# Kernel optimization log

Hardware: AMD Instinct MI355X
Metric: run time of the kernel (lower is better)

Reference implementation:

```python
import jax, jax.numpy as jnp
import numpy as np

KS = (16, 16, 16)  # k per layer

def _knn_idx(pts, k):
    # pts: (P, C). Exclude self (knn_graph default loop=False).
    P = pts.shape[0]
    sq = jnp.sum(pts * pts, axis=1)
    d2 = sq[:, None] + sq[None, :] - 2.0 * (pts @ pts.T)  # (P, P)
    d2 = d2.at[jnp.arange(P), jnp.arange(P)].set(jnp.inf)
    _, idx = jax.lax.top_k(-d2, k)  # (P, k) nearest neighbors
    return idx

def _edge_conv(h, idx, W, b):
    # h: (P, C); idx: (P, k); W: (2C, Cout)
    hi = h[:, None, :]                      # (P, 1, C)
    hj = h[idx]                             # (P, k, C) gather
    msg = jnp.concatenate([jnp.broadcast_to(hi, hj.shape), hj - hi], axis=-1)
    m = msg @ W + b                         # (P, k, Cout)
    return jnp.max(m, axis=1)               # max aggregation -> (P, Cout)

def setup_inputs() -> dict:
    key = jax.random.key(0)
    ks = jax.random.split(key, 12)
    B, N, d = 2, 4096, 3
    chans = [d, 64, 128, 256]
    inp = {"x": jax.random.normal(ks[0], (B, N, d), dtype=jnp.float32)}
    for i in range(3):
        cin, cout = chans[i], chans[i + 1]
        s = 1.0 / np.sqrt(2 * cin)
        inp[f"W{i+1}"] = jax.random.uniform(ks[1 + 2 * i], (2 * cin, cout), jnp.float32, -s, s)
        inp[f"b{i+1}"] = jax.random.uniform(ks[2 + 2 * i], (cout,), jnp.float32, -s, s)
    s1 = 1.0 / np.sqrt(256.0)
    inp["fW1"] = jax.random.uniform(ks[7], (256, 128), jnp.float32, -s1, s1)
    inp["fb1"] = jax.random.uniform(ks[8], (128,), jnp.float32, -s1, s1)
    s2 = 1.0 / np.sqrt(128.0)
    inp["fW2"] = jax.random.uniform(ks[9], (128, 1), jnp.float32, -s2, s2)
    inp["fb2"] = jax.random.uniform(ks[10], (1,), jnp.float32, -s2, s2)
    return inp

def reference(x, W1, b1, W2, b2, W3, b3, fW1, fb1, fW2, fb2):
    B, N, _ = x.shape
    h = x.reshape(B * N, -1)  # KNN spans flattened batch (batch=None in source)
    for (W, b, k) in ((W1, b1, KS[0]), (W2, b2, KS[1]), (W3, b3, KS[2])):
        idx = _knn_idx(h, k)
        h = jax.nn.relu(_edge_conv(h, idx, W, b))
    out = jax.nn.relu(h @ fW1 + fb1) @ fW2 + fb2  # (P, 1)
    return out.reshape(B, N, 1)
```

## Files before the change

kernel.cpp:

```cpp
#include <hip/hip_runtime.h>
#include <hip/hip_bf16.h>

#define PTS 8192
#define NSPLIT 8

__device__ __forceinline__ void top_init(float (&bd)[16], int (&bi)[16]) {
#pragma unroll
  for (int t = 0; t < 16; ++t) { bd[t] = 3e38f; bi[t] = 0; }
}

__device__ __forceinline__ void top_insert(float (&bd)[16], int (&bi)[16], float d, int j) {
  if (d < bd[15]) {
#pragma unroll
    for (int t = 15; t >= 0; --t) {
      bool c  = d < bd[t];
      bool cp = (t > 0) ? (d < bd[t - 1]) : false;
      float nd = cp ? bd[t - 1] : d;
      int   ni = cp ? bi[t - 1] : j;
      if (c) { bd[t] = nd; bi[t] = ni; }
    }
  }
}

__global__ void sqnorm_kernel(const float* __restrict__ h, float* __restrict__ sq, int C) {
  int i = blockIdx.x * 256 + threadIdx.x;
  if (i >= PTS) return;
  const float* r = h + (size_t)i * C;
  float s = 0.f;
  if ((C & 3) == 0) {
    for (int k = 0; k < C; k += 4) {
      float4 v = *(const float4*)(r + k);
      s += v.x * v.x + v.y * v.y + v.z * v.z + v.w * v.w;
    }
  } else {
    for (int k = 0; k < C; ++k) s += r[k] * r[k];
  }
  sq[i] = s;
}

template <int C>
__global__ __launch_bounds__(128) void knn_kernel(const float* __restrict__ H,
                                                  const float* __restrict__ sq,
                                                  float* __restrict__ pd,
                                                  int* __restrict__ pi) {
  constexpr int KC = (C < 16) ? C : 16;
  constexpr int NC = C / KC;
  constexpr int TT = (PTS / NSPLIT) / 64;
  constexpr int N  = TT * NC;

  __shared__ __align__(128) float AsF[C * 32];
  __shared__ __align__(128) float S[2048];

  const int tid  = threadIdx.x;
  const int b    = blockIdx.x;
  const int sy   = b & 7;
  const int sx   = b >> 3;
  const int row0 = sx * 32;
  const int cb   = sy * (PTS / NSPLIT);
  const int tx = tid & 15, ty = tid >> 4;
  const int r_ = tid & 31, g4 = tid >> 5;
  const int l_ = tid & 63, w_ = tid >> 6;

  if constexpr (C >= 16) {
    const int r = tid >> 2, q0 = tid & 3;
#pragma unroll
    for (int j = 0; j < C / 16; ++j) {
      int q = q0 + j * 4;
      float4 v = *(const float4*)(H + (size_t)(row0 + r) * C + q * 4);
      float vv[4] = {v.x, v.y, v.z, v.w};
#pragma unroll
      for (int e = 0; e < 4; ++e)
        AsF[(q * 4 + e) * 32 + r] = vv[e];
    }
  } else {
    if (tid < 32 * C) {
      int rr = tid & 31, kk = tid >> 5;
      AsF[kk * 32 + rr] = H[(size_t)(row0 + rr) * C + kk];
    }
  }

  float sqr[4];
#pragma unroll
  for (int u = 0; u < 4; ++u) sqr[u] = sq[row0 + ty * 4 + u];

  float bd[16]; int bi[16];
  top_init(bd, bi);

  float4 st0 = make_float4(0.f, 0.f, 0.f, 0.f);
  float4 st1 = make_float4(0.f, 0.f, 0.f, 0.f);
  auto stage_load = [&](int n1) {
    if constexpr (C >= 16) {
      const int c = tid & 63, kq = tid >> 6;
      const float* src = H + (size_t)(cb + (n1 / NC) * 64 + c) * C + (n1 % NC) * KC + kq * 8;
      st0 = *(const float4*)(src);
      st1 = *(const float4*)(src + 4);
    } else {
      if (tid < 64) {
        const float* src = H + (size_t)(cb + n1 * 64 + tid) * C;
        st0.x = src[0]; st0.y = src[1]; st0.z = src[2];
      }
    }
  };
  auto stage_write = [&](int n1) {
    float* B = S + (n1 & 1) * 1024;
    if constexpr (C >= 16) {
      const int c = tid & 63, kq = tid >> 6;
      float v0[4] = {st0.x, st0.y, st0.z, st0.w};
      float v1[4] = {st1.x, st1.y, st1.z, st1.w};
#pragma unroll
      for (int e = 0; e < 4; ++e) {
        B[(kq * 8 + e) * 64 + c]     = v0[e];
        B[(kq * 8 + 4 + e) * 64 + c] = v1[e];
      }
    } else {
      if (tid < 64) {
        B[0 * 64 + tid] = st0.x;
        B[1 * 64 + tid] = st0.y;
        B[2 * 64 + tid] = st0.z;
      }
    }
  };

  stage_load(0);
  stage_write(0);
  __syncthreads();

  float acc[4][4] = {};
  for (int n = 0; n < N; ++n) {
    if (n + 1 < N) stage_load(n + 1);
    const float* Bh = S + (n & 1) * 1024;
    const int kc = (n % NC) * KC;
#pragma unroll
    for (int k = 0; k < KC; ++k) {
      float4 a4 = *(const float4*)(AsF + (kc + k) * 32 + ty * 4);
      float4 b4 = *(const float4*)(Bh + k * 64 + tx * 4);
      float a[4]  = {a4.x, a4.y, a4.z, a4.w};
      float bb[4] = {b4.x, b4.y, b4.z, b4.w};
#pragma unroll
      for (int u = 0; u < 4; ++u)
#pragma unroll
        for (int v = 0; v < 4; ++v)
          acc[u][v] += a[u] * bb[v];
    }
    if ((n % NC) == NC - 1) {
      const int ct = (n / NC) * 64;
      const int cbase = cb + ct;
      float sqc[4];
#pragma unroll
      for (int v = 0; v < 4; ++v) sqc[v] = sq[cbase + tx * 4 + v];
      __syncthreads();
#pragma unroll
      for (int u = 0; u < 4; ++u) {
        int row = ty * 4 + u;
        int gr  = row0 + row;
        int sw  = (row & 7) << 2;
        float dv[4];
#pragma unroll
        for (int v = 0; v < 4; ++v) {
          float d2 = sqr[u] + sqc[v] - 2.f * acc[u][v];
          if (gr == cbase + tx * 4 + v) d2 = 3e38f;
          dv[v] = d2;
          acc[u][v] = 0.f;
        }
        *(float4*)(S + row * 64 + ((tx * 4) ^ sw)) = make_float4(dv[0], dv[1], dv[2], dv[3]);
      }
      __syncthreads();
      const int swr = (r_ & 7) << 2;
      unsigned mask = 0;
#pragma unroll
      for (int j = 0; j < 4; ++j) {
        float4 f = *(const float4*)(S + r_ * 64 + ((g4 * 16 + j * 4) ^ swr));
        if (f.x < bd[15]) mask |= (1u << (j * 4 + 0));
        if (f.y < bd[15]) mask |= (1u << (j * 4 + 1));
        if (f.z < bd[15]) mask |= (1u << (j * 4 + 2));
        if (f.w < bd[15]) mask |= (1u << (j * 4 + 3));
      }
      while (mask) {
        int q = __ffs(mask) - 1;
        mask &= mask - 1;
        int cc = g4 * 16 + q;
        float d = S[r_ * 64 + (cc ^ swr)];
        top_insert(bd, bi, d, cbase + cc);
      }
      __syncthreads();
    }
    if (n + 1 < N) {
      stage_write(n + 1);
      __syncthreads();
    }
  }

  for (int t = 0; t < 16; ++t) {
    float d = __shfl(bd[t], (l_ & 31) + 32);
    int   i = __shfl(bi[t], (l_ & 31) + 32);
    unsigned long long m = __ballot((l_ < 32) && (d < bd[15]));
    if (!m) break;
    if (l_ < 32) top_insert(bd, bi, d, i);
  }
  __syncthreads();
  if (w_ == 1 && l_ < 32) {
    float* base = S + r_ * 32;
#pragma unroll
    for (int t = 0; t < 16; ++t) {
      int s = (t + r_) & 15;
      base[s] = bd[t];
      ((int*)base)[16 + s] = bi[t];
    }
  }
  __syncthreads();
  if (w_ == 0 && l_ < 32) {
    const float* base = S + r_ * 32;
    for (int t = 0; t < 16; ++t) {
      int s = (t + r_) & 15;
      float d = base[s];
      if (d >= bd[15]) break;
      top_insert(bd, bi, d, ((const int*)base)[16 + s]);
    }
    size_t basep = ((size_t)(row0 + r_) * NSPLIT + sy) * 16;
#pragma unroll
    for (int t = 0; t < 16; ++t) { pd[basep + t] = bd[t]; pi[basep + t] = bi[t]; }
  }
}

__global__ void knn_merge_kernel(const float* __restrict__ pd, const int* __restrict__ pi,
                                 int* __restrict__ idx) {
  int i = blockIdx.x * 256 + threadIdx.x;
  if (i >= PTS) return;
  float bd[16]; int bi[16];
  top_init(bd, bi);
  const float* d  = pd + (size_t)i * (NSPLIT * 16);
  const int*   ii = pi + (size_t)i * (NSPLIT * 16);
  for (int L = 0; L < NSPLIT; ++L) {
    for (int t = 0; t < 16; ++t) {
      float dv = d[L * 16 + t];
      if (dv >= bd[15]) break;
      top_insert(bd, bi, dv, ii[L * 16 + t]);
    }
  }
#pragma unroll
  for (int t = 0; t < 16; ++t) idx[(size_t)i * 16 + t] = bi[t];
}

__global__ __launch_bounds__(256) void gemm_fg_kernel(const float* __restrict__ A,
                                                      const float* __restrict__ Wt,
                                                      const float* __restrict__ Wb,
                                                      const float* __restrict__ bias,
                                                      float* __restrict__ F, float* __restrict__ G,
                                                      int K, int N) {
  __shared__ float As[16][68];
  __shared__ float Bs[16][68];
  const int tid  = threadIdx.x;
  const int row0 = blockIdx.x * 64, col0 = blockIdx.y * 64;
  const float* B = (blockIdx.z == 0) ? Wt : Wb;
  float* O       = (blockIdx.z == 0) ? F  : G;
  const int tx = tid & 15, ty = tid >> 4;
  float acc[4][4] = {};
  for (int k0 = 0; k0 < K; k0 += 16) {
    __syncthreads();
#pragma unroll
    for (int l = 0; l < 4; ++l) {
      int rr = (tid >> 4) + l * 16, kk = tid & 15;
      As[kk][rr] = (k0 + kk < K) ? A[(size_t)(row0 + rr) * K + k0 + kk] : 0.f;
      int cc = tid & 63, k2 = (tid >> 6) + l * 4;
      Bs[k2][cc] = (k0 + k2 < K) ? B[(size_t)(k0 + k2) * N + col0 + cc] : 0.f;
    }
    __syncthreads();
#pragma unroll
    for (int k = 0; k < 16; ++k) {
      float4 a4 = *(const float4*)&As[k][ty * 4];
      float4 b4 = *(const float4*)&Bs[k][tx * 4];
      float a[4] = {a4.x, a4.y, a4.z, a4.w};
      float b[4] = {b4.x, b4.y, b4.z, b4.w};
#pragma unroll
      for (int u = 0; u < 4; ++u)
#pragma unroll
        for (int v = 0; v < 4; ++v)
          acc[u][v] += a[u] * b[v];
    }
  }
  float bv[4] = {0.f, 0.f, 0.f, 0.f};
  if (blockIdx.z == 0) {
#pragma unroll
    for (int v = 0; v < 4; ++v) bv[v] = bias[col0 + tx * 4 + v];
  }
#pragma unroll
  for (int u = 0; u < 4; ++u)
#pragma unroll
    for (int v = 0; v < 4; ++v)
      O[(size_t)(row0 + ty * 4 + u) * N + col0 + tx * 4 + v] = acc[u][v] + bv[v];
}

__global__ void gather_max_kernel(const float* __restrict__ F, const float* __restrict__ G,
                                  const int* __restrict__ idx, float* __restrict__ Ho, int Cn) {
  int t = blockIdx.x * 256 + threadIdx.x;
  int per = Cn >> 2;
  int i = t / per;
  if (i >= PTS) return;
  int c = (t - i * per) * 4;
  const int* ji = idx + (size_t)i * 16;
  float4 m = make_float4(-3e38f, -3e38f, -3e38f, -3e38f);
#pragma unroll
  for (int s = 0; s < 16; ++s) {
    float4 v = *(const float4*)(G + (size_t)ji[s] * Cn + c);
    m.x = fmaxf(m.x, v.x); m.y = fmaxf(m.y, v.y);
    m.z = fmaxf(m.z, v.z); m.w = fmaxf(m.w, v.w);
  }
  float4 gi = *(const float4*)(G + (size_t)i * Cn + c);
  float4 f  = *(const float4*)(F + (size_t)i * Cn + c);
  float4 o;
  o.x = fmaxf(f.x - gi.x + m.x, 0.f);
  o.y = fmaxf(f.y - gi.y + m.y, 0.f);
  o.z = fmaxf(f.z - gi.z + m.z, 0.f);
  o.w = fmaxf(f.w - gi.w + m.w, 0.f);
  *(float4*)(Ho + (size_t)i * Cn + c) = o;
}

__global__ __launch_bounds__(256) void mlp_kernel(const float* __restrict__ h3,
                                                  const float* __restrict__ fW1,
                                                  const float* __restrict__ fb1,
                                                  const float* __restrict__ fW2,
                                                  const float* __restrict__ fb2,
                                                  float* __restrict__ out) {
  __shared__ float hs[16][260];
  __shared__ float ws[64][128];
  __shared__ float red[4][8];
  const int tid = threadIdx.x;
  const int p0  = blockIdx.x * 16;
#pragma unroll
  for (int l = 0; l < 16; ++l) {
    int ii = l * 256 + tid;
    hs[ii >> 8][ii & 255] = h3[(size_t)(p0 + (ii >> 8)) * 256 + (ii & 255)];
  }
  const int c = tid & 127, half = tid >> 7;
  float acc[8];
#pragma unroll
  for (int pp = 0; pp < 8; ++pp) acc[pp] = fb1[c];
  for (int k0 = 0; k0 < 256; k0 += 64) {
    __syncthreads();
#pragma unroll
    for (int l = 0; l < 32; ++l) {
      int ii = l * 256 + tid;
      ws[ii >> 7][ii & 127] = fW1[(size_t)(k0 + (ii >> 7)) * 128 + (ii & 127)];
    }
    __syncthreads();
    for (int k = 0; k < 64; k += 4) {
      float w0 = ws[k][c], w1 = ws[k + 1][c], w2 = ws[k + 2][c], w3 = ws[k + 3][c];
#pragma unroll
      for (int pp = 0; pp < 8; ++pp) {
        float4 h4 = *(const float4*)&hs[half * 8 + pp][k0 + k];
        acc[pp] += h4.x * w0 + h4.y * w1 + h4.z * w2 + h4.w * w3;
      }
    }
  }
  float w2v = fW2[c];
  float s[8];
#pragma unroll
  for (int pp = 0; pp < 8; ++pp) s[pp] = fmaxf(acc[pp], 0.f) * w2v;
#pragma unroll
  for (int off = 32; off > 0; off >>= 1) {
#pragma unroll
    for (int pp = 0; pp < 8; ++pp) s[pp] += __shfl_down(s[pp], off);
  }
  if ((tid & 63) == 0) {
#pragma unroll
    for (int pp = 0; pp < 8; ++pp) red[tid >> 6][pp] = s[pp];
  }
  __syncthreads();
  if (tid < 16) {
    int hf = tid >> 3, pp = tid & 7;
    float v = red[hf * 2][pp] + red[hf * 2 + 1][pp] + fb2[0];
    out[p0 + hf * 8 + pp] = v;
  }
}

extern "C" void kernel_launch(void* const* d_in, const int* in_sizes, int n_in,
                              void* d_out, int out_size, void* d_ws, size_t ws_size,
                              hipStream_t stream) {
  (void)in_sizes; (void)n_in; (void)out_size; (void)ws_size;
  const float* x   = (const float*)d_in[0];
  const float* W1  = (const float*)d_in[1];
  const float* b1  = (const float*)d_in[2];
  const float* W2  = (const float*)d_in[3];
  const float* b2  = (const float*)d_in[4];
  const float* W3  = (const float*)d_in[5];
  const float* b3  = (const float*)d_in[6];
  const float* fW1 = (const float*)d_in[7];
  const float* fb1 = (const float*)d_in[8];
  const float* fW2 = (const float*)d_in[9];
  const float* fb2 = (const float*)d_in[10];

  float* w = (float*)d_ws;
  size_t o = 0;
  float* sq  = w + o; o += PTS;
  float* h1  = w + o; o += (size_t)PTS * 64;
  float* h2  = w + o; o += (size_t)PTS * 128;
  float* h3  = w + o; o += (size_t)PTS * 256;
  float* F   = w + o; o += (size_t)PTS * 256;
  float* G   = w + o; o += (size_t)PTS * 256;
  float* pd  = w + o; o += (size_t)PTS * 128;
  int*   pi  = (int*)(w + o); o += (size_t)PTS * 128;
  int*   idx = (int*)(w + o); o += (size_t)PTS * 16;

  const int KNN_GRID = (PTS / 32) * NSPLIT;

  sqnorm_kernel<<<PTS / 256, 256, 0, stream>>>(x, sq, 3);
  knn_kernel<3><<<KNN_GRID, 128, 0, stream>>>(x, sq, pd, pi);
  knn_merge_kernel<<<PTS / 256, 256, 0, stream>>>(pd, pi, idx);
  gemm_fg_kernel<<<dim3(PTS / 64, 1, 2), 256, 0, stream>>>(x, W1, W1 + 3 * 64, b1, F, G, 3, 64);
  gather_max_kernel<<<(PTS * 16 + 255) / 256, 256, 0, stream>>>(F, G, idx, h1, 64);

  sqnorm_kernel<<<PTS / 256, 256, 0, stream>>>(h1, sq, 64);
  knn_kernel<64><<<KNN_GRID, 128, 0, stream>>>(h1, sq, pd, pi);
  knn_merge_kernel<<<PTS / 256, 256, 0, stream>>>(pd, pi, idx);
  gemm_fg_kernel<<<dim3(PTS / 64, 2, 2), 256, 0, stream>>>(h1, W2, W2 + 64 * 128, b2, F, G, 64, 128);
  gather_max_kernel<<<(PTS * 32 + 255) / 256, 256, 0, stream>>>(F, G, idx, h2, 128);

  sqnorm_kernel<<<PTS / 256, 256, 0, stream>>>(h2, sq, 128);
  knn_kernel<128><<<KNN_GRID, 128, 0, stream>>>(h2, sq, pd, pi);
  knn_merge_kernel<<<PTS / 256, 256, 0, stream>>>(pd, pi, idx);
  gemm_fg_kernel<<<dim3(PTS / 64, 4, 2), 256, 0, stream>>>(h2, W3, W3 + 128 * 256, b3, F, G, 128, 256);
  gather_max_kernel<<<(PTS * 64 + 255) / 256, 256, 0, stream>>>(F, G, idx, h3, 256);

  mlp_kernel<<<PTS / 16, 256, 0, stream>>>(h3, fW1, fb1, fW2, fb2, (float*)d_out);
}
```

Baseline: 959.2 us.

## Compute KNN distance dot products with split-bf16 MFMA for layers 2 and 3

Adds a kernel that splits each fp32 feature into high and low bf16 parts, and a new KNN kernel that computes the pairwise dot products with four bf16 MFMA products per tile (hi·hi, hi·lo, lo·hi, lo·lo), approximating fp32 accuracy. Column tiles are double-buffered through shared memory, and distances pass through an LDS tile to the per-row top-16 insertion. The goal is to move the dominant pairwise-distance compute from FP32 ALU onto matrix cores. In exchange it adds a split pass and an extra buffer, and the emulated precision may slightly change neighbor ordering on near-ties.

```diff
diff --git a/kernel.cpp b/kernel.cpp
--- a/kernel.cpp
+++ b/kernel.cpp
@@ -3,6 +3,9 @@
 
 #define PTS 8192
 #define NSPLIT 8
+
+typedef __attribute__((ext_vector_type(8))) short bf16x8;
+typedef __attribute__((ext_vector_type(4))) float f32x4;
 
 __device__ __forceinline__ void top_init(float (&bd)[16], int (&bi)[16]) {
 #pragma unroll
@@ -36,6 +39,179 @@
     for (int k = 0; k < C; ++k) s += r[k] * r[k];
   }
   sq[i] = s;
+}
+
+__global__ void split_bf16_kernel(const float* __restrict__ h,
+                                  ushort* __restrict__ hi, ushort* __restrict__ lo, int n) {
+  int i = blockIdx.x * 256 + threadIdx.x;
+  if (i >= n) return;
+  float x = h[i];
+  unsigned u  = __float_as_uint(x);
+  unsigned hb = (u + 0x7FFFu + ((u >> 16) & 1u)) >> 16;
+  float hf = __uint_as_float(hb << 16);
+  float l  = x - hf;
+  unsigned ul = __float_as_uint(l);
+  unsigned lb = (ul + 0x7FFFu + ((ul >> 16) & 1u)) >> 16;
+  hi[i] = (ushort)hb;
+  lo[i] = (ushort)lb;
+}
+
+template <int C>
+__global__ __launch_bounds__(128) void knn_mfma_kernel(const ushort* __restrict__ Hhi,
+                                                       const ushort* __restrict__ Hlo,
+                                                       const float* __restrict__ sq,
+                                                       float* __restrict__ pd,
+                                                       int* __restrict__ pi) {
+  constexpr int NC = C / 32;
+  constexpr int TT = (PTS / NSPLIT) / 64;
+  constexpr int N  = TT * NC;
+
+  __shared__ __align__(128) ushort BsHi[2 * 2048];
+  __shared__ __align__(128) ushort BsLo[2 * 2048];
+  __shared__ __align__(128) float  D2F[32 * 68];
+
+  const int tid  = threadIdx.x;
+  const int b    = blockIdx.x;
+  const int sy   = b & 7;
+  const int sx   = b >> 3;
+  const int row0 = sx * 32;
+  const int cb   = sy * (PTS / NSPLIT);
+  const int l_ = tid & 63, w_ = tid >> 6;
+  const int r15 = l_ & 15, kg = l_ >> 4;
+  const int r_ = tid & 31, g4 = tid >> 5;
+
+  const int arow = row0 + w_ * 16 + r15;
+  bf16x8 ah[NC], al[NC];
+#pragma unroll
+  for (int c = 0; c < NC; ++c) {
+    ah[c] = *(const bf16x8*)(Hhi + (size_t)arow * C + c * 32 + kg * 8);
+    al[c] = *(const bf16x8*)(Hlo + (size_t)arow * C + c * 32 + kg * 8);
+  }
+
+  float sqr[4];
+#pragma unroll
+  for (int r = 0; r < 4; ++r) sqr[r] = sq[row0 + w_ * 16 + kg * 4 + r];
+
+  float bd[16]; int bi[16];
+  top_init(bd, bi);
+
+  f32x4 acc[4];
+#pragma unroll
+  for (int nb = 0; nb < 4; ++nb) acc[nb] = (f32x4){0.f, 0.f, 0.f, 0.f};
+
+  bf16x8 sh[2], sl[2];
+  auto stage_load = [&](int n1) {
+    const int ct = (n1 / NC) * 64, kc = (n1 % NC) * 32;
+#pragma unroll
+    for (int p = 0; p < 2; ++p) {
+      int e   = p * 1024 + tid * 8;
+      int col = e >> 5, k = e & 31;
+      size_t off = (size_t)(cb + ct + col) * C + kc + k;
+      sh[p] = *(const bf16x8*)(Hhi + off);
+      sl[p] = *(const bf16x8*)(Hlo + off);
+    }
+  };
+  auto stage_write = [&](int n1) {
+    ushort* BH = BsHi + (n1 & 1) * 2048;
+    ushort* BL = BsLo + (n1 & 1) * 2048;
+#pragma unroll
+    for (int p = 0; p < 2; ++p) {
+      int e = p * 1024 + tid * 8;
+      *(bf16x8*)(BH + e) = sh[p];
+      *(bf16x8*)(BL + e) = sl[p];
+    }
+  };
+
+  stage_load(0);
+  stage_write(0);
+  __syncthreads();
+
+  for (int n = 0; n < N; ++n) {
+    if (n + 1 < N) stage_load(n + 1);
+    const ushort* BH = BsHi + (n & 1) * 2048;
+    const ushort* BL = BsLo + (n & 1) * 2048;
+    const int cx = n % NC;
+#pragma unroll
+    for (int nb = 0; nb < 4; ++nb) {
+      int fo = (nb * 16 + r15) * 32 + kg * 8;
+      bf16x8 bh = *(const bf16x8*)(BH + fo);
+      bf16x8 bl = *(const bf16x8*)(BL + fo);
+      acc[nb] = __builtin_amdgcn_mfma_f32_16x16x32_bf16(ah[cx], bh, acc[nb], 0, 0, 0);
+      acc[nb] = __builtin_amdgcn_mfma_f32_16x16x32_bf16(ah[cx], bl, acc[nb], 0, 0, 0);
+      acc[nb] = __builtin_amdgcn_mfma_f32_16x16x32_bf16(al[cx], bh, acc[nb], 0, 0, 0);
+      acc[nb] = __builtin_amdgcn_mfma_f32_16x16x32_bf16(al[cx], bl, acc[nb], 0, 0, 0);
+    }
+    if (cx == NC - 1) {
+      const int ct = (n / NC) * 64;
+      const int cbase = cb + ct;
+#pragma unroll
+      for (int nb = 0; nb < 4; ++nb) {
+        int gc = cbase + nb * 16 + r15;
+        float sqc = sq[gc];
+#pragma unroll
+        for (int r = 0; r < 4; ++r) {
+          int row = w_ * 16 + kg * 4 + r;
+          float d2 = sqr[r] + sqc - 2.f * acc[nb][r];
+          if (row0 + row == gc) d2 = 3e38f;
+          D2F[row * 68 + nb * 16 + r15] = d2;
+        }
+        acc[nb] = (f32x4){0.f, 0.f, 0.f, 0.f};
+      }
+      __syncthreads();
+      unsigned mask = 0;
+#pragma unroll
+      for (int j = 0; j < 4; ++j) {
+        float4 f = *(const float4*)(D2F + r_ * 68 + g4 * 16 + j * 4);
+        if (f.x < bd[15]) mask |= (1u << (j * 4 + 0));
+        if (f.y < bd[15]) mask |= (1u << (j * 4 + 1));
+        if (f.z < bd[15]) mask |= (1u << (j * 4 + 2));
+        if (f.w < bd[15]) mask |= (1u << (j * 4 + 3));
+      }
+      while (mask) {
+        int q = __ffs(mask) - 1;
+        mask &= mask - 1;
+        int cc = g4 * 16 + q;
+        float d = D2F[r_ * 68 + cc];
+        top_insert(bd, bi, d, cbase + cc);
+      }
+      __syncthreads();
+    }
+    if (n + 1 < N) {
+      stage_write(n + 1);
+      __syncthreads();
+    }
+  }
+
+  for (int t = 0; t < 16; ++t) {
+    float d = __shfl(bd[t], (l_ & 31) + 32);
+    int   i = __shfl(bi[t], (l_ & 31) + 32);
+    unsigned long long m = __ballot((l_ < 32) && (d < bd[15]));
+    if (!m) break;
+    if (l_ < 32) top_insert(bd, bi, d, i);
+  }
+  __syncthreads();
+  if (w_ == 1 && l_ < 32) {
+    float* base = D2F + r_ * 32;
+#pragma unroll
+    for (int t = 0; t < 16; ++t) {
+      int s = (t + r_) & 15;
+      base[s] = bd[t];
+      ((int*)base)[16 + s] = bi[t];
+    }
+  }
+  __syncthreads();
+  if (w_ == 0 && l_ < 32) {
+    const float* base = D2F + r_ * 32;
+    for (int t = 0; t < 16; ++t) {
+      int s = (t + r_) & 15;
+      float d = base[s];
+      if (d >= bd[15]) break;
+      top_insert(bd, bi, d, ((const int*)base)[16 + s]);
+    }
+    size_t basep = ((size_t)(row0 + r_) * NSPLIT + sy) * 16;
+#pragma unroll
+    for (int t = 0; t < 16; ++t) { pd[basep + t] = bd[t]; pi[basep + t] = bi[t]; }
+  }
 }
 
 template <int C>
@@ -400,6 +576,8 @@
   float* pd  = w + o; o += (size_t)PTS * 128;
   int*   pi  = (int*)(w + o); o += (size_t)PTS * 128;
   int*   idx = (int*)(w + o); o += (size_t)PTS * 16;
+  ushort* hhi = (ushort*)(w + o); o += (size_t)PTS * 64;
+  ushort* hlo = (ushort*)(w + o); o += (size_t)PTS * 64;
 
   const int KNN_GRID = (PTS / 32) * NSPLIT;
 
@@ -410,13 +588,15 @@
   gather_max_kernel<<<(PTS * 16 + 255) / 256, 256, 0, stream>>>(F, G, idx, h1, 64);
 
   sqnorm_kernel<<<PTS / 256, 256, 0, stream>>>(h1, sq, 64);
-  knn_kernel<64><<<KNN_GRID, 128, 0, stream>>>(h1, sq, pd, pi);
+  split_bf16_kernel<<<(PTS * 64 + 255) / 256, 256, 0, stream>>>(h1, hhi, hlo, PTS * 64);
+  knn_mfma_kernel<64><<<KNN_GRID, 128, 0, stream>>>(hhi, hlo, sq, pd, pi);
   knn_merge_kernel<<<PTS / 256, 256, 0, stream>>>(pd, pi, idx);
   gemm_fg_kernel<<<dim3(PTS / 64, 2, 2), 256, 0, stream>>>(h1, W2, W2 + 64 * 128, b2, F, G, 64, 128);
   gather_max_kernel<<<(PTS * 32 + 255) / 256, 256, 0, stream>>>(F, G, idx, h2, 128);
 
   sqnorm_kernel<<<PTS / 256, 256, 0, stream>>>(h2, sq, 128);
-  knn_kernel<128><<<KNN_GRID, 128, 0, stream>>>(h2, sq, pd, pi);
+  split_bf16_kernel<<<(PTS * 128 + 255) / 256, 256, 0, stream>>>(h2, hhi, hlo, PTS * 128);
+  knn_mfma_kernel<128><<<KNN_GRID, 128, 0, stream>>>(hhi, hlo, sq, pd, pi);
   knn_merge_kernel<<<PTS / 256, 256, 0, stream>>>(pd, pi, idx);
   gemm_fg_kernel<<<dim3(PTS / 64, 4, 2), 256, 0, stream>>>(h2, W3, W3 + 128 * 256, b3, F, G, 128, 256);
   gather_max_kernel<<<(PTS * 64 + 255) / 256, 256, 0, stream>>>(F, G, idx, h3, 256);
```

Result: slower. 1.246 ms (+29.9%).
